# Performance work log

Hardware: AMD Instinct MI355X
Metric: run time of the kernel (lower is better)

Reference implementation:

```python
import jax, jax.numpy as jnp
import numpy as np

B, C = 2_000_000, 16


def setup_inputs() -> dict:
    key = jax.random.key(0)
    k1, k2 = jax.random.split(key)
    output = jax.random.normal(k1, (B, C), dtype=jnp.float32)
    score = jax.random.uniform(k2, (B,), dtype=jnp.float32)
    return {"output": output, "score": score}


def reference(output, score):
    # softmax over classes; top-1 value and index per row
    probs = jax.nn.softmax(output, axis=1)          # [B, C]
    prob_val = jnp.max(probs, axis=1)               # [B]
    prob_idx = jnp.argmax(probs, axis=1)            # [B]

    # select rows whose predicted top class is 0, preserving batch order.
    # jit-friendly: stable-sort selected rows to the front instead of boolean indexing.
    mask = prob_idx == 0                            # [B] bool
    order = jnp.argsort(jnp.logical_not(mask), stable=True)  # selected first, original order kept
    p = prob_val[order]                             # [B]
    s = score[order]                                # [B]
    n = jnp.sum(mask)                               # number of selected rows

    # adjacent-pair ranking loss over the first n entries:
    # sum_i log(1 + exp(-(p_i - p_{i+1}) * sign(s_i - s_{i+1})))
    tmp = (p[:-1] - p[1:]) * jnp.sign(s[:-1] - s[1:])        # [B-1]
    valid = jnp.arange(p.shape[0] - 1) < (n - 1)             # pairs fully inside selected prefix
    reg_term = jnp.sum(jnp.where(valid, jnp.log1p(jnp.exp(-tmp)), jnp.zeros_like(tmp)))
    return reg_term
```

## Files before the change

kernel.cpp:

```cpp
#include <hip/hip_runtime.h>

#define TPB 512
#define NW  (TPB / 64)

__device__ __forceinline__ float pair_loss(float p0, float s0, float p1, float s1) {
    float dp = p0 - p1;
    float ds = s0 - s1;
    float sg = (ds > 0.0f) ? 1.0f : ((ds < 0.0f) ? -1.0f : 0.0f);
    float t  = dp * sg;
    return fmaxf(-t, 0.0f) + log1pf(__expf(-fabsf(t)));
}

__device__ __forceinline__ void row_stats(const float* __restrict__ outp, int row,
                                          float& p, bool& mask) {
    const float4* o4 = (const float4*)outp + (size_t)row * 4;
    float4 a = o4[0];
    float4 b = o4[1];
    float4 c = o4[2];
    float4 d = o4[3];
    float m01 = fmaxf(fmaxf(a.x, a.y), fmaxf(a.z, a.w));
    float m23 = fmaxf(fmaxf(b.x, b.y), fmaxf(b.z, b.w));
    float m45 = fmaxf(fmaxf(c.x, c.y), fmaxf(c.z, c.w));
    float m67 = fmaxf(fmaxf(d.x, d.y), fmaxf(d.z, d.w));
    float m = fmaxf(fmaxf(m01, m23), fmaxf(m45, m67));
    float sum = __expf(a.x - m) + __expf(a.y - m) + __expf(a.z - m) + __expf(a.w - m)
              + __expf(b.x - m) + __expf(b.y - m) + __expf(b.z - m) + __expf(b.w - m)
              + __expf(c.x - m) + __expf(c.y - m) + __expf(c.z - m) + __expf(c.w - m)
              + __expf(d.x - m) + __expf(d.y - m) + __expf(d.z - m) + __expf(d.w - m);
    p = __builtin_amdgcn_rcpf(sum);
    mask = (a.x == m);
}

__global__ void __launch_bounds__(TPB) k_fused(const float* __restrict__ outp,
                                               const float* __restrict__ score,
                                               float* __restrict__ bpart, int B) {
    __shared__ float sp[TPB];
    __shared__ float ss[TPB];
    __shared__ unsigned long long wmask[NW];
    __shared__ float wsum[NW];

    int tid  = threadIdx.x;
    int lane = tid & 63;
    int wid  = tid >> 6;
    int row  = blockIdx.x * TPB + tid;

    bool mask = false;
    float p = 0.0f, s = 0.0f;
    if (row < B) {
        row_stats(outp, row, p, mask);
        s = score[row];
    }
    sp[tid] = p;
    ss[tid] = s;

    unsigned long long bal = __ballot(mask);
    if (lane == 0) wmask[wid] = bal;
    __syncthreads();

    float acc = 0.0f;
    if (mask) {
        unsigned long long above = bal & ~((2ull << lane) - 1ull);
        int nxt = -1;
        if (above) {
            nxt = (wid << 6) + __ffsll(above) - 1;
        } else {
            for (int w = wid + 1; w < NW; ++w)
                if (wmask[w]) { nxt = (w << 6) + __ffsll(wmask[w]) - 1; break; }
        }
        if (nxt >= 0) acc = pair_loss(p, s, sp[nxt], ss[nxt]);
    }

    if (wid == 0) {
        int last = -1;
        for (int w = NW - 1; w >= 0; --w)
            if (wmask[w]) { last = (w << 6) + 63 - __clzll(wmask[w]); break; }
        if (last >= 0) {
            float pl = sp[last];
            float sl = ss[last];
            int base = (blockIdx.x + 1) * TPB;
            while (base < B) {
                int r = base + lane;
                bool sel = false;
                float pf = 0.0f, sf = 0.0f;
                if (r < B) {
                    row_stats(outp, r, pf, sel);
                    sf = score[r];
                }
                unsigned long long b2 = __ballot(sel);
                if (b2) {
                    int fl = __ffsll(b2) - 1;
                    float pfirst = __shfl(pf, fl);
                    float sfirst = __shfl(sf, fl);
                    if (lane == 0) acc += pair_loss(pl, sl, pfirst, sfirst);
                    break;
                }
                base += 64;
            }
        }
    }

    for (int off = 32; off > 0; off >>= 1) acc += __shfl_down(acc, off);
    if (lane == 0) wsum[wid] = acc;
    __syncthreads();
    if (tid == 0) {
        float t = 0.0f;
        for (int w = 0; w < NW; ++w) t += wsum[w];
        bpart[blockIdx.x] = t;
    }
}

__global__ void k2_sum(const float* __restrict__ bpart, int nb,
                       float* __restrict__ out) {
    __shared__ float wsum[16];
    float acc = 0.0f;
    for (int b = threadIdx.x; b < nb; b += 1024) acc += bpart[b];
    int lane = threadIdx.x & 63;
    int wid  = threadIdx.x >> 6;
    for (int off = 32; off > 0; off >>= 1) acc += __shfl_down(acc, off);
    if (lane == 0) wsum[wid] = acc;
    __syncthreads();
    if (threadIdx.x == 0) {
        float t = 0.0f;
        for (int w = 0; w < 16; ++w) t += wsum[w];
        out[0] = t;
    }
}

extern "C" void kernel_launch(void* const* d_in, const int* in_sizes, int n_in,
                              void* d_out, int out_size, void* d_ws, size_t ws_size,
                              hipStream_t stream) {
    const float* outp  = (const float*)d_in[0];
    const float* score = (const float*)d_in[1];
    float* out = (float*)d_out;

    int B  = in_sizes[1];
    int nb = (B + TPB - 1) / TPB;

    float* bpart = (float*)d_ws;

    k_fused<<<nb, TPB, 0, stream>>>(outp, score, bpart, B);
    k2_sum<<<1, 1024, 0, stream>>>(bpart, nb, out);
}
```

Baseline: 31.52 us.

## Process four row chunks per block with register prefetch and carried boundary state

```diff
diff --git a/kernel.cpp b/kernel.cpp
--- a/kernel.cpp
+++ b/kernel.cpp
@@ -1,7 +1,9 @@
 #include <hip/hip_runtime.h>
 
-#define TPB 512
-#define NW  (TPB / 64)
+#define TPB   512
+#define CHUNK 4
+#define RPB   (TPB * CHUNK)
+#define NW    (TPB / 64)
 
 __device__ __forceinline__ float pair_loss(float p0, float s0, float p1, float s1) {
     float dp = p0 - p1;
@@ -11,13 +13,8 @@
     return fmaxf(-t, 0.0f) + log1pf(__expf(-fabsf(t)));
 }
 
-__device__ __forceinline__ void row_stats(const float* __restrict__ outp, int row,
-                                          float& p, bool& mask) {
-    const float4* o4 = (const float4*)outp + (size_t)row * 4;
-    float4 a = o4[0];
-    float4 b = o4[1];
-    float4 c = o4[2];
-    float4 d = o4[3];
+__device__ __forceinline__ void stats_from_regs(float4 a, float4 b, float4 c, float4 d,
+                                                float& p, bool& mask) {
     float m01 = fmaxf(fmaxf(a.x, a.y), fmaxf(a.z, a.w));
     float m23 = fmaxf(fmaxf(b.x, b.y), fmaxf(b.z, b.w));
     float m45 = fmaxf(fmaxf(c.x, c.y), fmaxf(c.z, c.w));
@@ -31,60 +28,103 @@
     mask = (a.x == m);
 }
 
+__device__ __forceinline__ void load_row(const float* __restrict__ outp,
+                                         const float* __restrict__ score,
+                                         int row, int B,
+                                         float4& a, float4& b, float4& c, float4& d,
+                                         float& s) {
+    if (row < B) {
+        const float4* o4 = (const float4*)outp + (size_t)row * 4;
+        a = o4[0]; b = o4[1]; c = o4[2]; d = o4[3];
+        s = score[row];
+    } else {
+        a = b = c = d = make_float4(0.f, 0.f, 0.f, 0.f);
+        s = 0.f;
+    }
+}
+
 __global__ void __launch_bounds__(TPB) k_fused(const float* __restrict__ outp,
                                                const float* __restrict__ score,
                                                float* __restrict__ bpart, int B) {
-    __shared__ float sp[TPB];
-    __shared__ float ss[TPB];
-    __shared__ unsigned long long wmask[NW];
+    __shared__ float sp[2][TPB];
+    __shared__ float ss[2][TPB];
+    __shared__ unsigned long long wmask[2][NW];
     __shared__ float wsum[NW];
 
     int tid  = threadIdx.x;
     int lane = tid & 63;
     int wid  = tid >> 6;
-    int row  = blockIdx.x * TPB + tid;
-
-    bool mask = false;
-    float p = 0.0f, s = 0.0f;
-    if (row < B) {
-        row_stats(outp, row, p, mask);
-        s = score[row];
-    }
-    sp[tid] = p;
-    ss[tid] = s;
-
-    unsigned long long bal = __ballot(mask);
-    if (lane == 0) wmask[wid] = bal;
-    __syncthreads();
+    int blk0 = blockIdx.x * RPB;
 
     float acc = 0.0f;
-    if (mask) {
-        unsigned long long above = bal & ~((2ull << lane) - 1ull);
-        int nxt = -1;
-        if (above) {
-            nxt = (wid << 6) + __ffsll(above) - 1;
-        } else {
-            for (int w = wid + 1; w < NW; ++w)
-                if (wmask[w]) { nxt = (w << 6) + __ffsll(wmask[w]) - 1; break; }
+    float cp = 0.0f, cs = 0.0f;
+    int   cvalid = 0;
+
+    float4 a0, b0, c0, d0, a1, b1, c1, d1;
+    float  s0, s1;
+    load_row(outp, score, blk0 + tid, B, a0, b0, c0, d0, s0);
+
+#pragma unroll
+    for (int t = 0; t < CHUNK; ++t) {
+        if (t + 1 < CHUNK)
+            load_row(outp, score, blk0 + (t + 1) * TPB + tid, B, a1, b1, c1, d1, s1);
+
+        float p; bool mask;
+        stats_from_regs(a0, b0, c0, d0, p, mask);
+        if (blk0 + t * TPB + tid >= B) mask = false;
+
+        int buf = t & 1;
+        sp[buf][tid] = p;
+        ss[buf][tid] = s0;
+        unsigned long long bal = __ballot(mask);
+        if (lane == 0) wmask[buf][wid] = bal;
+        __syncthreads();
+
+        if (mask) {
+            unsigned long long above = bal & ~((2ull << lane) - 1ull);
+            int nxt = -1;
+            if (above) {
+                nxt = (wid << 6) + __ffsll(above) - 1;
+            } else {
+                for (int w = wid + 1; w < NW; ++w)
+                    if (wmask[buf][w]) { nxt = (w << 6) + __ffsll(wmask[buf][w]) - 1; break; }
+            }
+            if (nxt >= 0) acc += pair_loss(p, s0, sp[buf][nxt], ss[buf][nxt]);
         }
-        if (nxt >= 0) acc = pair_loss(p, s, sp[nxt], ss[nxt]);
+
+        if (tid == 0) {
+            int first = -1, last = -1;
+            for (int w = 0; w < NW; ++w)
+                if (wmask[buf][w]) { first = (w << 6) + __ffsll(wmask[buf][w]) - 1; break; }
+            for (int w = NW - 1; w >= 0; --w)
+                if (wmask[buf][w]) { last = (w << 6) + 63 - __clzll(wmask[buf][w]); break; }
+            if (first >= 0) {
+                if (cvalid)
+                    acc += pair_loss(cp, cs, sp[buf][first], ss[buf][first]);
+                cp = sp[buf][last];
+                cs = ss[buf][last];
+                cvalid = 1;
+            }
+        }
+
+        a0 = a1; b0 = b1; c0 = c1; d0 = d1; s0 = s1;
     }
 
     if (wid == 0) {
-        int last = -1;
-        for (int w = NW - 1; w >= 0; --w)
-            if (wmask[w]) { last = (w << 6) + 63 - __clzll(wmask[w]); break; }
-        if (last >= 0) {
-            float pl = sp[last];
-            float sl = ss[last];
-            int base = (blockIdx.x + 1) * TPB;
+        int   v  = __shfl(cvalid, 0);
+        float pl = __shfl(cp, 0);
+        float sl = __shfl(cs, 0);
+        if (v) {
+            int base = blk0 + RPB;
             while (base < B) {
                 int r = base + lane;
                 bool sel = false;
                 float pf = 0.0f, sf = 0.0f;
                 if (r < B) {
-                    row_stats(outp, r, pf, sel);
-                    sf = score[r];
+                    float4 a, b, c, d; float sc;
+                    load_row(outp, score, r, B, a, b, c, d, sc);
+                    stats_from_regs(a, b, c, d, pf, sel);
+                    sf = sc;
                 }
                 unsigned long long b2 = __ballot(sel);
                 if (b2) {
@@ -111,9 +151,9 @@
 
 __global__ void k2_sum(const float* __restrict__ bpart, int nb,
                        float* __restrict__ out) {
-    __shared__ float wsum[16];
+    __shared__ float wsum[8];
     float acc = 0.0f;
-    for (int b = threadIdx.x; b < nb; b += 1024) acc += bpart[b];
+    for (int b = threadIdx.x; b < nb; b += 512) acc += bpart[b];
     int lane = threadIdx.x & 63;
     int wid  = threadIdx.x >> 6;
     for (int off = 32; off > 0; off >>= 1) acc += __shfl_down(acc, off);
@@ -121,7 +161,7 @@
     __syncthreads();
     if (threadIdx.x == 0) {
         float t = 0.0f;
-        for (int w = 0; w < 16; ++w) t += wsum[w];
+        for (int w = 0; w < 8; ++w) t += wsum[w];
         out[0] = t;
     }
 }
@@ -134,10 +174,10 @@
     float* out = (float*)d_out;
 
     int B  = in_sizes[1];
-    int nb = (B + TPB - 1) / TPB;
+    int nb = (B + RPB - 1) / RPB;
 
     float* bpart = (float*)d_ws;
 
     k_fused<<<nb, TPB, 0, stream>>>(outp, score, bpart, B);
-    k2_sum<<<1, 1024, 0, stream>>>(bpart, nb, out);
+    k2_sum<<<1, 512, 0, stream>>>(bpart, nb, out);
 }
```

After: 33.84 us. +7.4%, slower.

## Coalesce row loads with 4 lanes per row and shuffle-based softmax

Applied to the files above, without the earlier changes.

```diff
diff --git a/kernel.cpp b/kernel.cpp
--- a/kernel.cpp
+++ b/kernel.cpp
@@ -31,6 +31,10 @@
     mask = (a.x == m);
 }
 
+__device__ __forceinline__ unsigned int nib4(unsigned int x) {
+    return (((x & 0x1111u) * 0x1248u) >> 12) & 0xFu;
+}
+
 __global__ void __launch_bounds__(TPB) k_fused(const float* __restrict__ outp,
                                                const float* __restrict__ score,
                                                float* __restrict__ bpart, int B) {
@@ -42,20 +46,46 @@
     int tid  = threadIdx.x;
     int lane = tid & 63;
     int wid  = tid >> 6;
-    int row  = blockIdx.x * TPB + tid;
+    int wrow0 = blockIdx.x * TPB + (wid << 6);
 
-    bool mask = false;
-    float p = 0.0f, s = 0.0f;
-    if (row < B) {
-        row_stats(outp, row, p, mask);
-        s = score[row];
+    const float4* b4 = (const float4*)outp;
+    size_t f0   = (size_t)wrow0 * 4;
+    size_t fend = (size_t)B * 4;
+    float4 z = make_float4(0.f, 0.f, 0.f, 0.f);
+    float4 v0 = (f0 +   0 + lane < fend) ? b4[f0 +   0 + lane] : z;
+    float4 v1 = (f0 +  64 + lane < fend) ? b4[f0 +  64 + lane] : z;
+    float4 v2 = (f0 + 128 + lane < fend) ? b4[f0 + 128 + lane] : z;
+    float4 v3 = (f0 + 192 + lane < fend) ? b4[f0 + 192 + lane] : z;
+    float s = (wrow0 + lane < B) ? score[wrow0 + lane] : 0.0f;
+    ss[(wid << 6) + lane] = s;
+
+    unsigned long long mym = 0;
+#pragma unroll
+    for (int j = 0; j < 4; ++j) {
+        float4 x = (j == 0) ? v0 : (j == 1) ? v1 : (j == 2) ? v2 : v3;
+        float m = fmaxf(fmaxf(x.x, x.y), fmaxf(x.z, x.w));
+        m = fmaxf(m, __shfl_xor(m, 1));
+        m = fmaxf(m, __shfl_xor(m, 2));
+        float e = __expf(x.x - m) + __expf(x.y - m) + __expf(x.z - m) + __expf(x.w - m);
+        e += __shfl_xor(e, 1);
+        e += __shfl_xor(e, 2);
+        float x0 = __shfl(x.x, lane & ~3);
+        int rowlocal = (wid << 6) + (j << 4) + (lane >> 2);
+        bool msk = (x0 == m) && (blockIdx.x * TPB + rowlocal < B);
+        if ((lane & 3) == 0) sp[rowlocal] = __builtin_amdgcn_rcpf(e);
+        unsigned long long bal = __ballot(msk);
+        unsigned int lo = (unsigned int)bal, hi = (unsigned int)(bal >> 32);
+        unsigned int c = nib4(lo) | (nib4(lo >> 16) << 4)
+                       | (nib4(hi) << 8) | (nib4(hi >> 16) << 12);
+        mym |= (unsigned long long)c << (j << 4);
     }
-    sp[tid] = p;
-    ss[tid] = s;
+    if (lane == 0) wmask[wid] = mym;
+    __syncthreads();
 
-    unsigned long long bal = __ballot(mask);
-    if (lane == 0) wmask[wid] = bal;
-    __syncthreads();
+    unsigned long long bal = wmask[wid];
+    bool mask = (bal >> lane) & 1ull;
+    float p   = sp[tid];
+    float sc  = ss[tid];
 
     float acc = 0.0f;
     if (mask) {
@@ -67,7 +97,7 @@
             for (int w = wid + 1; w < NW; ++w)
                 if (wmask[w]) { nxt = (w << 6) + __ffsll(wmask[w]) - 1; break; }
         }
-        if (nxt >= 0) acc = pair_loss(p, s, sp[nxt], ss[nxt]);
+        if (nxt >= 0) acc = pair_loss(p, sc, sp[nxt], ss[nxt]);
     }
 
     if (wid == 0) {
@@ -77,7 +107,7 @@
         if (last >= 0) {
             float pl = sp[last];
             float sl = ss[last];
-            int base = (blockIdx.x + 1) * TPB;
+            int base = blockIdx.x * TPB + TPB;
             while (base < B) {
                 int r = base + lane;
                 bool sel = false;
```

After: 41.97 us. 1.33x slower.
